# Performance work log

Hardware: AMD Instinct MI355X
Metric: run time of the kernel (lower is better)

Reference implementation:

```python
import jax, jax.numpy as jnp
import numpy as np

B, C, HF, WF = 64, 512, 28, 28
HID = 512
NUM_CLS = 30
LOC_REG = 8
MAX_LEN = 500  # loop runs MAX_LEN + 1 = 501 steps


def setup_inputs() -> dict:
    key = jax.random.key(0)
    ks = jax.random.split(key, 12)
    sc = 0.02
    rn = lambda k, shape: jax.random.normal(k, shape, jnp.float32) * sc
    z = lambda shape: jnp.zeros(shape, jnp.float32)
    return {
        "fea": jax.random.normal(ks[0], (B, C, HF, WF), jnp.float32),
        # AttentionGRUCell params
        "i2h_w": rn(ks[1], (HID, C)),            # Linear(C, H, bias=False)
        "h2h_w": rn(ks[2], (HID, HID)),
        "h2h_b": z((HID,)),
        "score_w": rn(ks[3], (1, HID)),          # Linear(H, 1, bias=False)
        "gru_w_ih": rn(ks[4], (3 * HID, C + NUM_CLS)),
        "gru_w_hh": rn(ks[5], (3 * HID, HID)),
        "gru_b_ih": z((3 * HID,)),
        "gru_b_hh": z((3 * HID,)),
        # structure_generator: Linear(H,H) -> Linear(H, NUM_CLS) (no activation)
        "sg1_w": rn(ks[6], (HID, HID)), "sg1_b": z((HID,)),
        "sg2_w": rn(ks[7], (NUM_CLS, HID)), "sg2_b": z((NUM_CLS,)),
        # loc_generator: Linear(H,H) -> Linear(H, LOC_REG) -> Sigmoid
        "lg1_w": rn(ks[8], (HID, HID)), "lg1_b": z((HID,)),
        "lg2_w": rn(ks[9], (LOC_REG, HID)), "lg2_b": z((LOC_REG,)),
    }


def reference(fea, i2h_w, h2h_w, h2h_b, score_w, gru_w_ih, gru_w_hh,
              gru_b_ih, gru_b_hh, sg1_w, sg1_b, sg2_w, sg2_b,
              lg1_w, lg1_b, lg2_w, lg2_b):
    b = fea.shape[0]
    feat = fea.reshape(b, fea.shape[1], -1).transpose(0, 2, 1)      # [B, T, C]
    # i2h(batch_H) is step-invariant: hoist it out of the decode loop
    feat_proj = jnp.einsum('btc,hc->bth', feat, i2h_w)              # [B, T, H]
    sv = score_w[0]                                                  # [H]

    def gru_cell(x, h):
        gi = x @ gru_w_ih.T + gru_b_ih
        gh = h @ gru_w_hh.T + gru_b_hh
        i_r, i_z, i_n = jnp.split(gi, 3, axis=-1)
        h_r, h_z, h_n = jnp.split(gh, 3, axis=-1)
        r = jax.nn.sigmoid(i_r + h_r)
        z = jax.nn.sigmoid(i_z + h_z)
        n = jnp.tanh(i_n + r * h_n)
        return (1.0 - z) * n + z * h

    def step(carry, _):
        hidden, pre_chars = carry
        onehot = jax.nn.one_hot(pre_chars, NUM_CLS, dtype=feat.dtype)
        hproj = hidden @ h2h_w.T + h2h_b                             # [B, H]
        e = jnp.einsum('bth,h->bt', jnp.tanh(feat_proj + hproj[:, None, :]), sv)
        alpha = jax.nn.softmax(e, axis=1)                            # [B, T]
        context = jnp.einsum('bt,btc->bc', alpha, feat)              # [B, C]
        x = jnp.concatenate([context, onehot], axis=1)               # [B, C+NUM_CLS]
        new_hidden = gru_cell(x, hidden)
        structure_step = (new_hidden @ sg1_w.T + sg1_b) @ sg2_w.T + sg2_b
        loc_step = jax.nn.sigmoid((new_hidden @ lg1_w.T + lg1_b) @ lg2_w.T + lg2_b)
        new_chars = jnp.argmax(structure_step, axis=1)               # greedy decode
        return (new_hidden, new_chars), (structure_step, loc_step)

    hidden0 = jnp.zeros((b, HID), feat.dtype)
    chars0 = jnp.zeros((b,), jnp.int32)
    _, (structs, locs) = jax.lax.scan(step, (hidden0, chars0), None, length=MAX_LEN + 1)
    structure_probs = jax.nn.softmax(structs.transpose(1, 0, 2), axis=-1)  # eval-mode softmax
    loc_preds = locs.transpose(1, 0, 2)
    return structure_probs, loc_preds
```

## Files before the change

### kernel.cpp

```cpp
#include <hip/hip_runtime.h>
#include <hip/hip_bf16.h>


#define NB 64
#define TT 784
#define CC 512
#define HH 512
#define NCLS 30
#define LREG 8
#define STEPS 501
#define GRID_MAIN 256
#define THR_MAIN 1024

struct SlaP {
  __hip_bfloat16* feat16;
  __hip_bfloat16* fp16;
  float* hidT;
  float* hproj;
  float* h1sg;
  float* h1lg;
  float* ctxP;
  float* wsumP;
  int*   chars;
  unsigned* bar;
  const float *score_w, *w_ih, *w_hh, *b_ih, *b_hh;
  const float *h2h_w, *h2h_b, *sg1_w, *sg1_b, *sg2_w, *sg2_b;
  const float *lg1_w, *lg1_b, *lg2_w, *lg2_b;
  float *out_probs, *out_loc;
};

__device__ __forceinline__ float lo16(unsigned v){ return __uint_as_float(v << 16); }
__device__ __forceinline__ float hi16(unsigned v){ return __uint_as_float(v & 0xffff0000u); }

__device__ __forceinline__ float cld(const float* p){
  return __hip_atomic_load(p, __ATOMIC_RELAXED, __HIP_MEMORY_SCOPE_AGENT);
}
__device__ __forceinline__ void cst(float* p, float v){
  __hip_atomic_store(p, v, __ATOMIC_RELAXED, __HIP_MEMORY_SCOPE_AGENT);
}
__device__ __forceinline__ int cldi(const int* p){
  return __hip_atomic_load(p, __ATOMIC_RELAXED, __HIP_MEMORY_SCOPE_AGENT);
}
__device__ __forceinline__ void csti(int* p, int v){
  __hip_atomic_store(p, v, __ATOMIC_RELAXED, __HIP_MEMORY_SCOPE_AGENT);
}

__device__ __forceinline__ float tanh_fast(float x){
  float ex = __expf(2.f * x);
  return 1.f - 2.f * __builtin_amdgcn_rcpf(ex + 1.f);
}
__device__ __forceinline__ float sigmoid_fast(float x){
  return __builtin_amdgcn_rcpf(1.f + __expf(-x));
}
__device__ __forceinline__ float warp_sum(float v){
  #pragma unroll
  for (int m = 32; m > 0; m >>= 1) v += __shfl_xor(v, m, 64);
  return v;
}
__device__ __forceinline__ float warp_max(float v){
  #pragma unroll
  for (int m = 32; m > 0; m >>= 1) v = fmaxf(v, __shfl_xor(v, m, 64));
  return v;
}
__device__ __forceinline__ int warp_min_i(int v){
  #pragma unroll
  for (int m = 32; m > 0; m >>= 1) v = min(v, __shfl_xor(v, m, 64));
  return v;
}

__device__ __forceinline__ void gbar(unsigned* bar, unsigned target){
  __syncthreads();
  if (threadIdx.x == 0){
    unsigned* c8 = bar + 8 + (blockIdx.x & 7) * 32;
    unsigned p = __hip_atomic_fetch_add(c8, 1u, __ATOMIC_RELAXED, __HIP_MEMORY_SCOPE_AGENT);
    if (p == 32u * target - 1u){
      unsigned pm = __hip_atomic_fetch_add(bar, 1u, __ATOMIC_RELAXED, __HIP_MEMORY_SCOPE_AGENT);
      if (pm == 8u * target - 1u)
        __hip_atomic_store(bar + 64, target, __ATOMIC_RELAXED, __HIP_MEMORY_SCOPE_AGENT);
    }
    while (__hip_atomic_load(bar + 64, __ATOMIC_RELAXED, __HIP_MEMORY_SCOPE_AGENT) < target)
      __builtin_amdgcn_s_sleep(1);
  }
  __syncthreads();
}


__global__ void k_init(SlaP p){
  int idx = blockIdx.x * blockDim.x + threadIdx.x;
  if (idx < 512*64) p.hidT[idx] = 0.f;
  if (idx < 64*512) p.hproj[idx] = p.h2h_b[idx & 511];
  if (idx < 64) p.chars[idx] = 0;
  if (idx < 512) p.bar[idx] = 0u;
}

__global__ void k_transpose(const float* __restrict__ fea, __hip_bfloat16* __restrict__ feat16){
  __shared__ float tile[64][65];
  const int b = blockIdx.z, t0 = blockIdx.x * 64, c0 = blockIdx.y * 64;
  #pragma unroll
  for (int r = 0; r < 16; ++r){
    int idx = threadIdx.x + 256*r;
    int ci = idx >> 6, tj = idx & 63;
    float v = 0.f;
    if (t0 + tj < TT) v = fea[((size_t)b*CC + (c0+ci))*TT + t0 + tj];
    tile[ci][tj] = v;
  }
  __syncthreads();
  #pragma unroll
  for (int r = 0; r < 16; ++r){
    int idx = threadIdx.x + 256*r;
    int tj = idx >> 6, ci = idx & 63;
    if (t0 + tj < TT)
      feat16[((size_t)b*TT + t0 + tj)*CC + c0 + ci] = __float2bfloat16(tile[ci][tj]);
  }
}

__global__ void k_fpgemm(const float* __restrict__ fea, const float* __restrict__ i2h,
                         __hip_bfloat16* __restrict__ fp16){
  const int b = blockIdx.z, t0 = blockIdx.x * 64, h0 = blockIdx.y * 64;
  const int tx = threadIdx.x & 15, ty = threadIdx.x >> 4;
  const int tb = t0 + tx*4, hb = h0 + ty*4;
  const int ts = (tb < TT) ? tb : 0;
  const float* A = fea + (size_t)b*CC*TT;
  float acc[4][4];
  #pragma unroll
  for (int j = 0; j < 4; ++j)
    #pragma unroll
    for (int i2 = 0; i2 < 4; ++i2) acc[j][i2] = 0.f;
  for (int k = 0; k < CC; ++k){
    const float4 a4 = *(const float4*)&A[(size_t)k*TT + ts];
    float bv0 = i2h[(size_t)(hb+0)*CC + k];
    float bv1 = i2h[(size_t)(hb+1)*CC + k];
    float bv2 = i2h[(size_t)(hb+2)*CC + k];
    float bv3 = i2h[(size_t)(hb+3)*CC + k];
    acc[0][0] += bv0*a4.x; acc[0][1] += bv0*a4.y; acc[0][2] += bv0*a4.z; acc[0][3] += bv0*a4.w;
    acc[1][0] += bv1*a4.x; acc[1][1] += bv1*a4.y; acc[1][2] += bv1*a4.z; acc[1][3] += bv1*a4.w;
    acc[2][0] += bv2*a4.x; acc[2][1] += bv2*a4.y; acc[2][2] += bv2*a4.z; acc[2][3] += bv2*a4.w;
    acc[3][0] += bv3*a4.x; acc[3][1] += bv3*a4.y; acc[3][2] += bv3*a4.z; acc[3][3] += bv3*a4.w;
  }
  if (tb < TT){
    #pragma unroll
    for (int j = 0; j < 4; ++j)
      #pragma unroll
      for (int i2 = 0; i2 < 4; ++i2)
        fp16[((size_t)b*TT + tb + i2)*CC + hb + j] = __float2bfloat16(acc[j][i2]);
  }
}


__global__ void __launch_bounds__(THR_MAIN, 4) sla_main(SlaP p){
  const int tid  = threadIdx.x;
  const int lane = tid & 63;
  const int wv   = tid >> 6;
  const int blk  = blockIdx.x;
  __shared__ float sm[12352];
  float* smF = sm + 12288;

  const int ab = blk >> 2;
  const int aslice = blk & 3;
  float svr[8];
  #pragma unroll
  for (int k = 0; k < 8; ++k) svr[k] = p.score_w[lane*8 + k];

  unsigned bid = 0;

  for (int i = 0; i <= STEPS; ++i){
    if (i > 0 && blk < NB){
      const int fb = blk;
      for (int task = wv; task < 38; task += 16){
        const float* wrow; const float* src; float bias;
        if (task < 30){ wrow = p.sg2_w + task*512; bias = p.sg2_b[task]; src = p.h1sg + fb*512; }
        else          { wrow = p.lg2_w + (task-30)*512; bias = p.lg2_b[task-30]; src = p.h1lg + fb*512; }
        float s = 0.f;
        #pragma unroll
        for (int k = 0; k < 8; ++k) s += wrow[lane + 64*k] * cld(&src[lane + 64*k]);
        s = warp_sum(s);
        if (task < 30){ if (lane == 0) smF[task] = s + bias; }
        else if (lane == 0)
          p.out_loc[(size_t)fb*(STEPS*LREG) + (size_t)(i-1)*LREG + (task-30)] = sigmoid_fast(s + bias);
      }
    }
    __syncthreads();
    if (i > 0 && blk < NB && wv == 0){
      float sv_ = (lane < 30) ? smF[lane] : -3.4e38f;
      float m = warp_max(sv_);
      float e = (lane < 30) ? __expf(sv_ - m) : 0.f;
      float ssum = warp_sum(e);
      if (lane < 30)
        p.out_probs[(size_t)blk*(STEPS*NCLS) + (size_t)(i-1)*NCLS + lane] = e / ssum;
      int cand = (lane < 30 && sv_ == m) ? lane : 1000;
      cand = warp_min_i(cand);
      if (lane == 0) csti(&p.chars[blk], cand);
    }
    if (i == STEPS) break;
    {
      float hpr[8];
      #pragma unroll
      for (int k = 0; k < 8; ++k) hpr[k] = cld(&p.hproj[ab*512 + lane*8 + k]);
      float acc[8] = {0,0,0,0,0,0,0,0};
      float wsr = 0.f;
      const int tl0 = aslice * 196;
      const unsigned short* fpB = (const unsigned short*)p.fp16 + ((size_t)ab*TT)*512;
      const unsigned short* ftB = (const unsigned short*)p.feat16 + ((size_t)ab*TT)*512;
      const int rc = (wv < 4) ? 13 : 12;
      size_t rowo = (size_t)(tl0 + wv)*512 + lane*8;
      uint4 pf = *(const uint4*)(fpB + rowo);
      uint4 pt = *(const uint4*)(ftB + rowo);
      for (int r = 0; r < rc; ++r){
        const uint4 cf = pf, ct = pt;
        if (r + 1 < rc){
          rowo += (size_t)16*512;
          pf = *(const uint4*)(fpB + rowo);
          pt = *(const uint4*)(ftB + rowo);
        }
        float e0 = 0.f, x;
        x = lo16(cf.x)+hpr[0]; e0 += tanh_fast(x)*svr[0];
        x = hi16(cf.x)+hpr[1]; e0 += tanh_fast(x)*svr[1];
        x = lo16(cf.y)+hpr[2]; e0 += tanh_fast(x)*svr[2];
        x = hi16(cf.y)+hpr[3]; e0 += tanh_fast(x)*svr[3];
        x = lo16(cf.z)+hpr[4]; e0 += tanh_fast(x)*svr[4];
        x = hi16(cf.z)+hpr[5]; e0 += tanh_fast(x)*svr[5];
        x = lo16(cf.w)+hpr[6]; e0 += tanh_fast(x)*svr[6];
        x = hi16(cf.w)+hpr[7]; e0 += tanh_fast(x)*svr[7];
        e0 = warp_sum(e0);
        float wgt = __expf(e0);
        acc[0] += wgt*lo16(ct.x); acc[1] += wgt*hi16(ct.x);
        acc[2] += wgt*lo16(ct.y); acc[3] += wgt*hi16(ct.y);
        acc[4] += wgt*lo16(ct.z); acc[5] += wgt*hi16(ct.z);
        acc[6] += wgt*lo16(ct.w); acc[7] += wgt*hi16(ct.w);
        wsr += wgt;
      }
      if (wv < 8){
        #pragma unroll
        for (int k = 0; k < 8; ++k) sm[wv*512 + lane*8 + k] = acc[k];
      }
      if (lane == 0) smF[32 + wv] = wsr;
      __syncthreads();
      if (wv >= 8){
        #pragma unroll
        for (int k = 0; k < 8; ++k) sm[(wv-8)*512 + lane*8 + k] += acc[k];
      }
      __syncthreads();
      if (tid < 512){
        float s = 0.f;
        #pragma unroll
        for (int r = 0; r < 8; ++r) s += sm[r*512 + tid];
        cst(&p.ctxP[((size_t)aslice*512 + tid)*64 + ab], s);
      } else if (tid == 512){
        float s = 0.f;
        #pragma unroll
        for (int r = 0; r < 16; ++r) s += smF[32 + r];
        cst(&p.wsumP[aslice*64 + ab], s);
      }
    }
    gbar(p.bar, ++bid);
    if (blk < 128){
      const int j0 = blk * 4;
      const float* hidC = p.hidT + (i & 1)*(512*64);
      float accI[4][3], accH[4][3];
      #pragma unroll
      for (int jj = 0; jj < 4; ++jj)
        #pragma unroll
        for (int g = 0; g < 3; ++g){ accI[jj][g] = 0.f; accH[jj][g] = 0.f; }
      const int kb = wv * 32;
      for (int kk = 0; kk < 32; kk += 4){
        const int k = kb + kk;
        float xv[4], hv[4];
        #pragma unroll
        for (int t = 0; t < 4; ++t){
          float s = 0.f;
          #pragma unroll
          for (int sl = 0; sl < 4; ++sl) s += cld(&p.ctxP[((size_t)sl*512 + k + t)*64 + lane]);
          xv[t] = s;
          hv[t] = cld(&hidC[(k + t)*64 + lane]);
        }
        #pragma unroll
        for (int jj = 0; jj < 4; ++jj)
          #pragma unroll
          for (int g = 0; g < 3; ++g){
            const int row = g*512 + j0 + jj;
            const float4 wi = *(const float4*)&p.w_ih[(size_t)row*542 + k];
            const float4 wh = *(const float4*)&p.w_hh[(size_t)row*512 + k];
            accI[jj][g] += wi.x*xv[0] + wi.y*xv[1] + wi.z*xv[2] + wi.w*xv[3];
            accH[jj][g] += wh.x*hv[0] + wh.y*hv[1] + wh.z*hv[2] + wh.w*hv[3];
          }
      }
      const int slot = wv & 7;
      if (wv < 8){
        #pragma unroll
        for (int jj = 0; jj < 4; ++jj)
          #pragma unroll
          for (int g = 0; g < 3; ++g){
            sm[((slot*24) + jj*6 + g    )*64 + lane] = accI[jj][g];
            sm[((slot*24) + jj*6 + 3 + g)*64 + lane] = accH[jj][g];
          }
      }
      __syncthreads();
      if (wv >= 8){
        #pragma unroll
        for (int jj = 0; jj < 4; ++jj)
          #pragma unroll
          for (int g = 0; g < 3; ++g){
            sm[((slot*24) + jj*6 + g    )*64 + lane] += accI[jj][g];
            sm[((slot*24) + jj*6 + 3 + g)*64 + lane] += accH[jj][g];
          }
      }
      __syncthreads();
      if (tid < 256){
        const int jj = tid >> 6, b = tid & 63;
        float ws = 0.f;
        #pragma unroll
        for (int sl = 0; sl < 4; ++sl) ws += cld(&p.wsumP[sl*64 + b]);
        const float inv = 1.f / ws;
        const int ch = cldi(&p.chars[b]);
        float gi[3], gh[3];
        #pragma unroll
        for (int g = 0; g < 3; ++g){
          float giS = 0.f, ghS = 0.f;
          #pragma unroll
          for (int sl = 0; sl < 8; ++sl){
            giS += sm[((sl*24) + jj*6 + g    )*64 + b];
            ghS += sm[((sl*24) + jj*6 + 3 + g)*64 + b];
          }
          const int row = g*512 + j0 + jj;
          gi[g] = giS*inv + p.w_ih[(size_t)row*542 + 512 + ch] + p.b_ih[row];
          gh[g] = ghS + p.b_hh[row];
        }
        float r_ = sigmoid_fast(gi[0] + gh[0]);
        float z_ = sigmoid_fast(gi[1] + gh[1]);
        float n_ = tanh_fast(gi[2] + r_*gh[2]);
        float hold = cld(&hidC[(j0 + jj)*64 + b]);
        cst(&p.hidT[((i+1) & 1)*(512*64) + (j0 + jj)*64 + b], (1.f - z_)*n_ + z_*hold);
      }
    } else {
      __syncthreads();
    }
    gbar(p.bar, ++bid);
    if (blk < 128){
      const int r0 = blk * 12;
      const float* hidN = p.hidT + ((i+1) & 1)*(512*64);
      const float* rowp[12];
      #pragma unroll
      for (int r = 0; r < 12; ++r){
        const int rg = r0 + r, head = rg >> 9, j = rg & 511;
        const float* base = (head == 0) ? p.h2h_w : (head == 1) ? p.sg1_w : p.lg1_w;
        rowp[r] = base + (size_t)j*512;
      }
      float acc[12];
      #pragma unroll
      for (int r = 0; r < 12; ++r) acc[r] = 0.f;
      const int kb = wv * 32;
      for (int kk = 0; kk < 32; kk += 4){
        const int k = kb + kk;
        float hv[4];
        #pragma unroll
        for (int t = 0; t < 4; ++t) hv[t] = cld(&hidN[(k + t)*64 + lane]);
        #pragma unroll
        for (int r = 0; r < 12; ++r){
          const float4 w4 = *(const float4*)&rowp[r][k];
          acc[r] += w4.x*hv[0] + w4.y*hv[1] + w4.z*hv[2] + w4.w*hv[3];
        }
      }
      const int slot = wv & 7;
      if (wv < 8){
        #pragma unroll
        for (int r = 0; r < 12; ++r) sm[((slot*12) + r)*64 + lane] = acc[r];
      }
      __syncthreads();
      if (wv >= 8){
        #pragma unroll
        for (int r = 0; r < 12; ++r) sm[((slot*12) + r)*64 + lane] += acc[r];
      }
      __syncthreads();
      if (tid < 768){
        const int r = tid >> 6, b = tid & 63;
        float s = 0.f;
        #pragma unroll
        for (int sl = 0; sl < 8; ++sl) s += sm[((sl*12) + r)*64 + b];
        const int rg = r0 + r, head = rg >> 9, j = rg & 511;
        const float bias = (head == 0) ? p.h2h_b[j] : (head == 1) ? p.sg1_b[j] : p.lg1_b[j];
        float* dst = (head == 0) ? p.hproj : (head == 1) ? p.h1sg : p.h1lg;
        cst(&dst[b*512 + j], s + bias);
      }
    } else {
      __syncthreads(); __syncthreads();
    }
    gbar(p.bar, ++bid);
  }
}

extern "C" void kernel_launch(void* const* d_in, const int* in_sizes, int n_in,
                              void* d_out, int out_size, void* d_ws, size_t ws_size,
                              hipStream_t stream){
  (void)in_sizes; (void)n_in; (void)out_size; (void)ws_size;
  char* w = (char*)d_ws;
  size_t off = 0;
  auto carve = [&](size_t bytes) -> char* {
    char* r = w + off; off += (bytes + 255) & ~(size_t)255; return r;
  };
  SlaP p;
  p.feat16 = (__hip_bfloat16*)carve((size_t)NB*TT*CC*2);
  p.fp16   = (__hip_bfloat16*)carve((size_t)NB*TT*HH*2);
  p.hidT   = (float*)carve((size_t)2*512*64*4);
  p.hproj  = (float*)carve((size_t)64*512*4);
  p.h1sg   = (float*)carve((size_t)64*512*4);
  p.h1lg   = (float*)carve((size_t)64*512*4);
  p.ctxP   = (float*)carve((size_t)4*512*64*4);
  p.wsumP  = (float*)carve(4*64*4);
  p.chars  = (int*)carve(64*4);
  p.bar    = (unsigned*)carve(2048);

  p.score_w = (const float*)d_in[4];
  p.w_ih  = (const float*)d_in[5];  p.w_hh  = (const float*)d_in[6];
  p.b_ih  = (const float*)d_in[7];  p.b_hh  = (const float*)d_in[8];
  p.h2h_w = (const float*)d_in[2];  p.h2h_b = (const float*)d_in[3];
  p.sg1_w = (const float*)d_in[9];  p.sg1_b = (const float*)d_in[10];
  p.sg2_w = (const float*)d_in[11]; p.sg2_b = (const float*)d_in[12];
  p.lg1_w = (const float*)d_in[13]; p.lg1_b = (const float*)d_in[14];
  p.lg2_w = (const float*)d_in[15]; p.lg2_b = (const float*)d_in[16];
  p.out_probs = (float*)d_out;
  p.out_loc   = p.out_probs + (size_t)NB*STEPS*NCLS;

  const float* fea = (const float*)d_in[0];
  const float* i2h = (const float*)d_in[1];

  k_init<<<128, 256, 0, stream>>>(p);
  k_transpose<<<dim3(13, 8, 64), 256, 0, stream>>>(fea, p.feat16);
  k_fpgemm<<<dim3(13, 8, 64), 256, 0, stream>>>(fea, i2h, p.fp16);
  sla_main<<<GRID_MAIN, THR_MAIN, 0, stream>>>(p);
}
```

Before: 47.27 ms.

## Pair-interleave hidden/context buffers, reduce context via atomics, process two rows per iteration

Hidden state and context buffers are re-laid out as interleaved float pairs so coherent loads and stores can move 64-bit values instead of single floats. The four per-slice context and weight-sum partials are replaced by float atomic adds into one buffer, which idle blocks zero in a later phase. The attention loop now handles two timestep rows per iteration with a paired warp reduction, and the GRU and projection epilogues each write two outputs per thread. This is meant to cut global traffic latency and shuffle overhead on the serial decode path, at the cost of atomic contention, nondeterministic summation order and a zeroing step that depends on barrier ordering.

```diff
diff --git a/kernel.cpp b/kernel.cpp
--- a/kernel.cpp
+++ b/kernel.cpp
@@ -15,12 +15,12 @@
 struct SlaP {
   __hip_bfloat16* feat16;
   __hip_bfloat16* fp16;
-  float* hidT;
+  float* hid2;
   float* hproj;
   float* h1sg;
   float* h1lg;
-  float* ctxP;
-  float* wsumP;
+  float* ctx2;
+  float* wsum;
   int*   chars;
   unsigned* bar;
   const float *score_w, *w_ih, *w_hh, *b_ih, *b_hh;
@@ -44,6 +44,16 @@
 __device__ __forceinline__ void csti(int* p, int v){
   __hip_atomic_store(p, v, __ATOMIC_RELAXED, __HIP_MEMORY_SCOPE_AGENT);
 }
+__device__ __forceinline__ float2 cld2(const float* p){
+  unsigned long long v = __hip_atomic_load((const unsigned long long*)p,
+                          __ATOMIC_RELAXED, __HIP_MEMORY_SCOPE_AGENT);
+  union { unsigned long long u; float2 f; } c; c.u = v; return c.f;
+}
+__device__ __forceinline__ void cst2(float* p, float a, float b){
+  union { unsigned long long u; float2 f; } c; c.f = make_float2(a, b);
+  __hip_atomic_store((unsigned long long*)p, c.u,
+                     __ATOMIC_RELAXED, __HIP_MEMORY_SCOPE_AGENT);
+}
 
 __device__ __forceinline__ float tanh_fast(float x){
   float ex = __expf(2.f * x);
@@ -56,6 +66,14 @@
   #pragma unroll
   for (int m = 32; m > 0; m >>= 1) v += __shfl_xor(v, m, 64);
   return v;
+}
+__device__ __forceinline__ void warp_sum2(float& a, float& b){
+  #pragma unroll
+  for (int m = 32; m > 0; m >>= 1){
+    float ta = __shfl_xor(a, m, 64);
+    float tb = __shfl_xor(b, m, 64);
+    a += ta; b += tb;
+  }
 }
 __device__ __forceinline__ float warp_max(float v){
   #pragma unroll
@@ -87,9 +105,9 @@
 
 __global__ void k_init(SlaP p){
   int idx = blockIdx.x * blockDim.x + threadIdx.x;
-  if (idx < 512*64) p.hidT[idx] = 0.f;
+  if (idx < 32768){ p.hid2[idx] = 0.f; p.ctx2[idx] = 0.f; }
   if (idx < 64*512) p.hproj[idx] = p.h2h_b[idx & 511];
-  if (idx < 64) p.chars[idx] = 0;
+  if (idx < 64){ p.wsum[idx] = 0.f; p.chars[idx] = 0; }
   if (idx < 512) p.bar[idx] = 0u;
 }
 
@@ -172,7 +190,11 @@
         else          { wrow = p.lg2_w + (task-30)*512; bias = p.lg2_b[task-30]; src = p.h1lg + fb*512; }
         float s = 0.f;
         #pragma unroll
-        for (int k = 0; k < 8; ++k) s += wrow[lane + 64*k] * cld(&src[lane + 64*k]);
+        for (int kq = 0; kq < 4; ++kq){
+          const float2 wv2 = *(const float2*)&wrow[lane*2 + 128*kq];
+          const float2 sv2 = cld2(&src[lane*2 + 128*kq]);
+          s += wv2.x*sv2.x + wv2.y*sv2.y;
+        }
         s = warp_sum(s);
         if (task < 30){ if (lane == 0) smF[task] = s + bias; }
         else if (lane == 0)
@@ -195,39 +217,79 @@
     {
       float hpr[8];
       #pragma unroll
-      for (int k = 0; k < 8; ++k) hpr[k] = cld(&p.hproj[ab*512 + lane*8 + k]);
+      for (int k = 0; k < 4; ++k){
+        float2 h2 = cld2(&p.hproj[ab*512 + lane*8 + 2*k]);
+        hpr[2*k] = h2.x; hpr[2*k+1] = h2.y;
+      }
       float acc[8] = {0,0,0,0,0,0,0,0};
       float wsr = 0.f;
       const int tl0 = aslice * 196;
       const unsigned short* fpB = (const unsigned short*)p.fp16 + ((size_t)ab*TT)*512;
       const unsigned short* ftB = (const unsigned short*)p.feat16 + ((size_t)ab*TT)*512;
-      const int rc = (wv < 4) ? 13 : 12;
-      size_t rowo = (size_t)(tl0 + wv)*512 + lane*8;
-      uint4 pf = *(const uint4*)(fpB + rowo);
-      uint4 pt = *(const uint4*)(ftB + rowo);
-      for (int r = 0; r < rc; ++r){
-        const uint4 cf = pf, ct = pt;
-        if (r + 1 < rc){
-          rowo += (size_t)16*512;
-          pf = *(const uint4*)(fpB + rowo);
-          pt = *(const uint4*)(ftB + rowo);
+      const int cnt = (wv < 4) ? 13 : 12;
+      const int r0r = wv*12 + ((wv < 4) ? wv : 4);
+      const unsigned short* fpR = fpB + (size_t)(tl0 + r0r)*512 + lane*8;
+      const unsigned short* ftR = ftB + (size_t)(tl0 + r0r)*512 + lane*8;
+      uint4 f0 = *(const uint4*)(fpR);
+      uint4 g0 = *(const uint4*)(ftR);
+      uint4 f1 = *(const uint4*)(fpR + 512);
+      uint4 g1 = *(const uint4*)(ftR + 512);
+      const int np = cnt >> 1;
+      for (int pi = 0; pi < np; ++pi){
+        const uint4 cf0 = f0, cg0 = g0, cf1 = f1, cg1 = g1;
+        fpR += 1024; ftR += 1024;
+        if (pi + 1 < np){
+          f0 = *(const uint4*)(fpR);       g0 = *(const uint4*)(ftR);
+          f1 = *(const uint4*)(fpR + 512); g1 = *(const uint4*)(ftR + 512);
+        } else if (cnt & 1){
+          f0 = *(const uint4*)(fpR);       g0 = *(const uint4*)(ftR);
         }
+        float ea = 0.f, eb = 0.f, x;
+        x = lo16(cf0.x)+hpr[0]; ea += tanh_fast(x)*svr[0];
+        x = lo16(cf1.x)+hpr[0]; eb += tanh_fast(x)*svr[0];
+        x = hi16(cf0.x)+hpr[1]; ea += tanh_fast(x)*svr[1];
+        x = hi16(cf1.x)+hpr[1]; eb += tanh_fast(x)*svr[1];
+        x = lo16(cf0.y)+hpr[2]; ea += tanh_fast(x)*svr[2];
+        x = lo16(cf1.y)+hpr[2]; eb += tanh_fast(x)*svr[2];
+        x = hi16(cf0.y)+hpr[3]; ea += tanh_fast(x)*svr[3];
+        x = hi16(cf1.y)+hpr[3]; eb += tanh_fast(x)*svr[3];
+        x = lo16(cf0.z)+hpr[4]; ea += tanh_fast(x)*svr[4];
+        x = lo16(cf1.z)+hpr[4]; eb += tanh_fast(x)*svr[4];
+        x = hi16(cf0.z)+hpr[5]; ea += tanh_fast(x)*svr[5];
+        x = hi16(cf1.z)+hpr[5]; eb += tanh_fast(x)*svr[5];
+        x = lo16(cf0.w)+hpr[6]; ea += tanh_fast(x)*svr[6];
+        x = lo16(cf1.w)+hpr[6]; eb += tanh_fast(x)*svr[6];
+        x = hi16(cf0.w)+hpr[7]; ea += tanh_fast(x)*svr[7];
+        x = hi16(cf1.w)+hpr[7]; eb += tanh_fast(x)*svr[7];
+        warp_sum2(ea, eb);
+        const float wa = __expf(ea), wb = __expf(eb);
+        acc[0] += wa*lo16(cg0.x) + wb*lo16(cg1.x);
+        acc[1] += wa*hi16(cg0.x) + wb*hi16(cg1.x);
+        acc[2] += wa*lo16(cg0.y) + wb*lo16(cg1.y);
+        acc[3] += wa*hi16(cg0.y) + wb*hi16(cg1.y);
+        acc[4] += wa*lo16(cg0.z) + wb*lo16(cg1.z);
+        acc[5] += wa*hi16(cg0.z) + wb*hi16(cg1.z);
+        acc[6] += wa*lo16(cg0.w) + wb*lo16(cg1.w);
+        acc[7] += wa*hi16(cg0.w) + wb*hi16(cg1.w);
+        wsr += wa + wb;
+      }
+      if (cnt & 1){
         float e0 = 0.f, x;
-        x = lo16(cf.x)+hpr[0]; e0 += tanh_fast(x)*svr[0];
-        x = hi16(cf.x)+hpr[1]; e0 += tanh_fast(x)*svr[1];
-        x = lo16(cf.y)+hpr[2]; e0 += tanh_fast(x)*svr[2];
-        x = hi16(cf.y)+hpr[3]; e0 += tanh_fast(x)*svr[3];
-        x = lo16(cf.z)+hpr[4]; e0 += tanh_fast(x)*svr[4];
-        x = hi16(cf.z)+hpr[5]; e0 += tanh_fast(x)*svr[5];
-        x = lo16(cf.w)+hpr[6]; e0 += tanh_fast(x)*svr[6];
-        x = hi16(cf.w)+hpr[7]; e0 += tanh_fast(x)*svr[7];
+        x = lo16(f0.x)+hpr[0]; e0 += tanh_fast(x)*svr[0];
+        x = hi16(f0.x)+hpr[1]; e0 += tanh_fast(x)*svr[1];
+        x = lo16(f0.y)+hpr[2]; e0 += tanh_fast(x)*svr[2];
+        x = hi16(f0.y)+hpr[3]; e0 += tanh_fast(x)*svr[3];
+        x = lo16(f0.z)+hpr[4]; e0 += tanh_fast(x)*svr[4];
+        x = hi16(f0.z)+hpr[5]; e0 += tanh_fast(x)*svr[5];
+        x = lo16(f0.w)+hpr[6]; e0 += tanh_fast(x)*svr[6];
+        x = hi16(f0.w)+hpr[7]; e0 += tanh_fast(x)*svr[7];
         e0 = warp_sum(e0);
-        float wgt = __expf(e0);
-        acc[0] += wgt*lo16(ct.x); acc[1] += wgt*hi16(ct.x);
-        acc[2] += wgt*lo16(ct.y); acc[3] += wgt*hi16(ct.y);
-        acc[4] += wgt*lo16(ct.z); acc[5] += wgt*hi16(ct.z);
-        acc[6] += wgt*lo16(ct.w); acc[7] += wgt*hi16(ct.w);
-        wsr += wgt;
+        const float wa = __expf(e0);
+        acc[0] += wa*lo16(g0.x); acc[1] += wa*hi16(g0.x);
+        acc[2] += wa*lo16(g0.y); acc[3] += wa*hi16(g0.y);
+        acc[4] += wa*lo16(g0.z); acc[5] += wa*hi16(g0.z);
+        acc[6] += wa*lo16(g0.w); acc[7] += wa*hi16(g0.w);
+        wsr += wa;
       }
       if (wv < 8){
         #pragma unroll
@@ -244,18 +306,18 @@
         float s = 0.f;
         #pragma unroll
         for (int r = 0; r < 8; ++r) s += sm[r*512 + tid];
-        cst(&p.ctxP[((size_t)aslice*512 + tid)*64 + ab], s);
+        unsafeAtomicAdd(&p.ctx2[(tid >> 1)*128 + ab*2 + (tid & 1)], s);
       } else if (tid == 512){
         float s = 0.f;
         #pragma unroll
         for (int r = 0; r < 16; ++r) s += smF[32 + r];
-        cst(&p.wsumP[aslice*64 + ab], s);
+        unsafeAtomicAdd(&p.wsum[ab], s);
       }
     }
     gbar(p.bar, ++bid);
     if (blk < 128){
       const int j0 = blk * 4;
-      const float* hidC = p.hidT + (i & 1)*(512*64);
+      const float* hidC = p.hid2 + (i & 1)*(512*64);
       float accI[4][3], accH[4][3];
       #pragma unroll
       for (int jj = 0; jj < 4; ++jj)
@@ -264,15 +326,10 @@
       const int kb = wv * 32;
       for (int kk = 0; kk < 32; kk += 4){
         const int k = kb + kk;
-        float xv[4], hv[4];
-        #pragma unroll
-        for (int t = 0; t < 4; ++t){
-          float s = 0.f;
-          #pragma unroll
-          for (int sl = 0; sl < 4; ++sl) s += cld(&p.ctxP[((size_t)sl*512 + k + t)*64 + lane]);
-          xv[t] = s;
-          hv[t] = cld(&hidC[(k + t)*64 + lane]);
-        }
+        const float2 x01 = cld2(&p.ctx2[(k >> 1)*128 + lane*2]);
+        const float2 x23 = cld2(&p.ctx2[(k >> 1)*128 + 128 + lane*2]);
+        const float2 h01 = cld2(&hidC[(k >> 1)*128 + lane*2]);
+        const float2 h23 = cld2(&hidC[(k >> 1)*128 + 128 + lane*2]);
         #pragma unroll
         for (int jj = 0; jj < 4; ++jj)
           #pragma unroll
@@ -280,8 +337,8 @@
             const int row = g*512 + j0 + jj;
             const float4 wi = *(const float4*)&p.w_ih[(size_t)row*542 + k];
             const float4 wh = *(const float4*)&p.w_hh[(size_t)row*512 + k];
-            accI[jj][g] += wi.x*xv[0] + wi.y*xv[1] + wi.z*xv[2] + wi.w*xv[3];
-            accH[jj][g] += wh.x*hv[0] + wh.y*hv[1] + wh.z*hv[2] + wh.w*hv[3];
+            accI[jj][g] += wi.x*x01.x + wi.y*x01.y + wi.z*x23.x + wi.w*x23.y;
+            accH[jj][g] += wh.x*h01.x + wh.y*h01.y + wh.z*h23.x + wh.w*h23.y;
           }
       }
       const int slot = wv & 7;
@@ -305,39 +362,46 @@
           }
       }
       __syncthreads();
-      if (tid < 256){
-        const int jj = tid >> 6, b = tid & 63;
+      if (tid < 128){
+        const int pp = tid >> 6;
+        const int b = tid & 63;
         float ws = 0.f;
-        #pragma unroll
-        for (int sl = 0; sl < 4; ++sl) ws += cld(&p.wsumP[sl*64 + b]);
+        ws = cld(&p.wsum[b]);
         const float inv = 1.f / ws;
         const int ch = cldi(&p.chars[b]);
-        float gi[3], gh[3];
-        #pragma unroll
-        for (int g = 0; g < 3; ++g){
-          float giS = 0.f, ghS = 0.f;
+        const float2 ho = cld2(&hidC[((j0 >> 1) + pp)*128 + b*2]);
+        float nh[2];
+        #pragma unroll
+        for (int q = 0; q < 2; ++q){
+          const int jj = pp*2 + q;
+          float gi[3], gh[3];
           #pragma unroll
-          for (int sl = 0; sl < 8; ++sl){
-            giS += sm[((sl*24) + jj*6 + g    )*64 + b];
-            ghS += sm[((sl*24) + jj*6 + 3 + g)*64 + b];
+          for (int g = 0; g < 3; ++g){
+            float giS = 0.f, ghS = 0.f;
+            #pragma unroll
+            for (int sl = 0; sl < 8; ++sl){
+              giS += sm[((sl*24) + jj*6 + g    )*64 + b];
+              ghS += sm[((sl*24) + jj*6 + 3 + g)*64 + b];
+            }
+            const int row = g*512 + j0 + jj;
+            gi[g] = giS*inv + p.w_ih[(size_t)row*542 + 512 + ch] + p.b_ih[row];
+            gh[g] = ghS + p.b_hh[row];
           }
-          const int row = g*512 + j0 + jj;
-          gi[g] = giS*inv + p.w_ih[(size_t)row*542 + 512 + ch] + p.b_ih[row];
-          gh[g] = ghS + p.b_hh[row];
+          float r_ = sigmoid_fast(gi[0] + gh[0]);
+          float z_ = sigmoid_fast(gi[1] + gh[1]);
+          float n_ = tanh_fast(gi[2] + r_*gh[2]);
+          float hold = (q == 0) ? ho.x : ho.y;
+          nh[q] = (1.f - z_)*n_ + z_*hold;
         }
-        float r_ = sigmoid_fast(gi[0] + gh[0]);
-        float z_ = sigmoid_fast(gi[1] + gh[1]);
-        float n_ = tanh_fast(gi[2] + r_*gh[2]);
-        float hold = cld(&hidC[(j0 + jj)*64 + b]);
-        cst(&p.hidT[((i+1) & 1)*(512*64) + (j0 + jj)*64 + b], (1.f - z_)*n_ + z_*hold);
+        cst2(&p.hid2[((i+1) & 1)*(512*64) + ((j0 >> 1) + pp)*128 + b*2], nh[0], nh[1]);
       }
     } else {
-      __syncthreads();
+      __syncthreads(); __syncthreads();
     }
     gbar(p.bar, ++bid);
     if (blk < 128){
       const int r0 = blk * 12;
-      const float* hidN = p.hidT + ((i+1) & 1)*(512*64);
+      const float* hidN = p.hid2 + ((i+1) & 1)*(512*64);
       const float* rowp[12];
       #pragma unroll
       for (int r = 0; r < 12; ++r){
@@ -351,13 +415,12 @@
       const int kb = wv * 32;
       for (int kk = 0; kk < 32; kk += 4){
         const int k = kb + kk;
-        float hv[4];
-        #pragma unroll
-        for (int t = 0; t < 4; ++t) hv[t] = cld(&hidN[(k + t)*64 + lane]);
+        const float2 h01 = cld2(&hidN[(k >> 1)*128 + lane*2]);
+        const float2 h23 = cld2(&hidN[(k >> 1)*128 + 128 + lane*2]);
         #pragma unroll
         for (int r = 0; r < 12; ++r){
           const float4 w4 = *(const float4*)&rowp[r][k];
-          acc[r] += w4.x*hv[0] + w4.y*hv[1] + w4.z*hv[2] + w4.w*hv[3];
+          acc[r] += w4.x*h01.x + w4.y*h01.y + w4.z*h23.x + w4.w*h23.y;
         }
       }
       const int slot = wv & 7;
@@ -371,17 +434,23 @@
         for (int r = 0; r < 12; ++r) sm[((slot*12) + r)*64 + lane] += acc[r];
       }
       __syncthreads();
-      if (tid < 768){
-        const int r = tid >> 6, b = tid & 63;
-        float s = 0.f;
-        #pragma unroll
-        for (int sl = 0; sl < 8; ++sl) s += sm[((sl*12) + r)*64 + b];
-        const int rg = r0 + r, head = rg >> 9, j = rg & 511;
-        const float bias = (head == 0) ? p.h2h_b[j] : (head == 1) ? p.sg1_b[j] : p.lg1_b[j];
+      if (tid < 384){
+        const int q = tid >> 6, b = tid & 63;
+        float s0 = 0.f, s1 = 0.f;
+        #pragma unroll
+        for (int sl = 0; sl < 8; ++sl){
+          s0 += sm[((sl*12) + 2*q    )*64 + b];
+          s1 += sm[((sl*12) + 2*q + 1)*64 + b];
+        }
+        const int rg = r0 + 2*q, head = rg >> 9, j = rg & 511;
+        const float* bb = (head == 0) ? p.h2h_b : (head == 1) ? p.sg1_b : p.lg1_b;
         float* dst = (head == 0) ? p.hproj : (head == 1) ? p.h1sg : p.h1lg;
-        cst(&dst[b*512 + j], s + bias);
+        cst2(&dst[b*512 + j], s0 + bb[j], s1 + bb[j+1]);
       }
     } else {
+      const int bz = blk - 128;
+      if (tid < 256) cst(&p.ctx2[bz*256 + tid], 0.f);
+      if (bz == 127 && tid < 64) cst(&p.wsum[tid], 0.f);
       __syncthreads(); __syncthreads();
     }
     gbar(p.bar, ++bid);
@@ -400,12 +469,12 @@
   SlaP p;
   p.feat16 = (__hip_bfloat16*)carve((size_t)NB*TT*CC*2);
   p.fp16   = (__hip_bfloat16*)carve((size_t)NB*TT*HH*2);
-  p.hidT   = (float*)carve((size_t)2*512*64*4);
+  p.hid2   = (float*)carve((size_t)2*512*64*4);
   p.hproj  = (float*)carve((size_t)64*512*4);
   p.h1sg   = (float*)carve((size_t)64*512*4);
   p.h1lg   = (float*)carve((size_t)64*512*4);
-  p.ctxP   = (float*)carve((size_t)4*512*64*4);
-  p.wsumP  = (float*)carve(4*64*4);
+  p.ctx2   = (float*)carve((size_t)512*64*4);
+  p.wsum   = (float*)carve(64*4);
   p.chars  = (int*)carve(64*4);
   p.bar    = (unsigned*)carve(2048);
 
```

Result: faster. 38.80 ms (-17.9%).
